# Optimization experiments

Hardware: AMD Instinct MI355X
Metric: run time of the kernel (lower is better)

Reference implementation:

```python
import jax, jax.numpy as jnp
import numpy as np
from jax import lax


def setup_inputs() -> dict:
    key = jax.random.key(0)
    kx, kw = jax.random.split(key)
    x = jax.random.normal(kx, (8, 32, 16, 160, 160), dtype=jnp.float32)
    # xavier-normal-ish init (scale irrelevant to correctness testing)
    weights = jax.random.normal(kw, (32, 32, 1, 3, 3), dtype=jnp.float32) * 0.1
    return {"x": x, "weights": weights}


def reference(x, weights):
    # per-(out_ch, in_ch) scale: mean |w| over kernel dims (2,3,4), detached
    scale = lax.stop_gradient(jnp.mean(jnp.abs(weights), axis=(2, 3, 4), keepdims=True))
    binary_no_grad = scale * jnp.sign(weights)          # {+-scale}
    clipped = jnp.clip(weights, -1.0, 1.0)
    # straight-through estimator: value = binary_no_grad, grad flows via clipped
    binary_weights = lax.stop_gradient(binary_no_grad - clipped) + clipped
    out = lax.conv_general_dilated(
        x, binary_weights,
        window_strides=(1, 1, 1),
        padding=((0, 0), (1, 1), (1, 1)),
        rhs_dilation=(1, 1, 1),
        dimension_numbers=("NCDHW", "OIDHW", "NCDHW"),
        feature_group_count=1,
    )
    return out
```

## Files before the change

kernel.cpp:

```cpp
#include <hip/hip_runtime.h>


typedef _Float16 half8 __attribute__((ext_vector_type(8)));
typedef float    floatx4 __attribute__((ext_vector_type(4)));

#define DHW  409600
#define HW   25600

__global__ void bnn_wprep_kernel(const float* __restrict__ w,
                                 _Float16* __restrict__ ws) {
    const int tid = threadIdx.x;
    #pragma unroll
    for (int p4 = 0; p4 < 4; ++p4) {
        const int oi = tid * 4 + p4;
        const int o  = oi >> 5;
        const int i  = oi & 31;
        const float* wp = w + oi * 9;
        float s = 0.f;
        #pragma unroll
        for (int t = 0; t < 9; ++t) s += fabsf(wp[t]);
        s *= (1.f / 9.f);
        const int l = ((i >> 3) << 4) | (o & 15);
        const int p = o >> 4;
        const int j = i & 7;
        #pragma unroll
        for (int t = 0; t < 9; ++t) {
            const float v  = wp[t];
            const float sg = (v > 0.f) ? 1.f : ((v < 0.f) ? -1.f : 0.f);
            ws[((t * 2 + p) * 64 + l) * 8 + j] = (_Float16)(s * sg);
        }
    }
}

__global__ __launch_bounds__(512, 4) void bnn_conv3d_kernel(
        const float* __restrict__ x, const _Float16* __restrict__ ws,
        float* __restrict__ out) {
    __shared__ __align__(16) _Float16 ldsh[31104];

    const int tid  = threadIdx.x;
    const int lane = tid & 63;
    const int wid  = tid >> 6;

    const int bid = blockIdx.x;
    const int ht  = bid % 40;
    const int nd  = bid / 40;
    const int d   = nd & 15;
    const int n   = nd >> 4;
    const int h0  = ht * 4;

    float xv[8][8];
    #pragma unroll
    for (int it = 0; it < 8; ++it) {
        const bool active = (it < 7) || (tid < 256);
        const int idx  = it * 512 + tid;
        const int wpos = idx % 160;
        const int rest = idx / 160;
        const int kg   = rest & 3;
        const int r    = rest >> 2;
        const int h_in = h0 - 1 + r;
        if (active && (unsigned)h_in < 160u) {
            const float* src = x + ((n * 32 + kg * 8) * 16 + d) * HW
                                 + h_in * 160 + wpos;
            #pragma unroll
            for (int c = 0; c < 8; ++c) xv[it][c] = src[c * DHW];
        } else {
            #pragma unroll
            for (int c = 0; c < 8; ++c) xv[it][c] = 0.f;
        }
    }

    if (tid < 192) {
        const int pos = tid >> 4, word = tid & 15;
        const int r   = pos >> 1;
        const int w1  = (pos & 1) ? 161 : 0;
        reinterpret_cast<unsigned int*>(ldsh)[(r * 162 + w1) * 16 + word] = 0u;
    }

    #pragma unroll
    for (int it = 0; it < 8; ++it) {
        const bool active = (it < 7) || (tid < 256);
        if (active) {
            const int idx  = it * 512 + tid;
            const int wpos = idx % 160;
            const int rest = idx / 160;
            const int kg   = rest & 3;
            const int r    = rest >> 2;
            half8 pk;
            #pragma unroll
            for (int c = 0; c < 8; ++c) pk[c] = (_Float16)xv[it][c];
            const int w1  = wpos + 1;
            const int skg = kg ^ ((w1 >> 1) & 3);
            *reinterpret_cast<half8*>(&ldsh[(r * 162 + w1) * 32 + skg * 8]) = pk;
        }
    }
    __syncthreads();

    half8 wf[2][9];
    {
        const half8* fb = reinterpret_cast<const half8*>(ws);
        #pragma unroll
        for (int t = 0; t < 9; ++t) {
            wf[0][t] = fb[(t * 2 + 0) * 64 + lane];
            wf[1][t] = fb[(t * 2 + 1) * 64 + lane];
        }
    }

    const int s16   = lane & 15;
    const int kg    = lane >> 4;
    const int row   = wid & 3;
    const int whalf = wid >> 2;
    const int h     = h0 + row;
    const int obase = (n * 32 + s16) * DHW + d * HW + h * 160 + kg * 4;

    #pragma unroll
    for (int wtl = 0; wtl < 5; ++wtl) {
        const int wbase = (whalf * 5 + wtl) * 16;
        floatx4 acc0 = {0.f, 0.f, 0.f, 0.f};
        floatx4 acc1 = {0.f, 0.f, 0.f, 0.f};
        #pragma unroll
        for (int kh = 0; kh < 3; ++kh) {
            const int rrow = (row + kh) * 162;
            #pragma unroll
            for (int kw = 0; kw < 3; ++kw) {
                const int w1   = wbase + s16 + kw;
                const int aidx = (rrow + w1) * 32 + ((kg ^ ((w1 >> 1) & 3)) * 8);
                const half8 a  = *reinterpret_cast<const half8*>(&ldsh[aidx]);
                const int t = kh * 3 + kw;
                acc0 = __builtin_amdgcn_mfma_f32_16x16x32_f16(a, wf[0][t], acc0, 0, 0, 0);
                acc1 = __builtin_amdgcn_mfma_f32_16x16x32_f16(a, wf[1][t], acc1, 0, 0, 0);
            }
        }
        float* op = out + obase + wbase;
        *reinterpret_cast<floatx4*>(op)            = acc0;
        *reinterpret_cast<floatx4*>(op + 16 * DHW) = acc1;
    }
}

extern "C" void kernel_launch(void* const* d_in, const int* in_sizes, int n_in,
                              void* d_out, int out_size, void* d_ws, size_t ws_size,
                              hipStream_t stream) {
    const float* x = (const float*)d_in[0];
    const float* w = (const float*)d_in[1];
    float* out = (float*)d_out;
    _Float16* ws = (_Float16*)d_ws;
    bnn_wprep_kernel<<<dim3(1), dim3(256), 0, stream>>>(w, ws);
    bnn_conv3d_kernel<<<dim3(5120), dim3(512), 0, stream>>>(x, ws, out);
}
```

Baseline: 229.0 us.

## Vectorize input loads to float4 and re-swizzle LDS layout for conflict-free writes

Each thread now loads 4 consecutive w positions per channel with float4 global loads (2 items per thread instead of 8 scalar groups), then writes 4 half8 vectors to LDS. The LDS swizzle gains an extra XOR on the w index to avoid bank conflicts from the new write pattern. Weight fragment loads move before the barrier so they overlap with the staging, and the MFMA loop is reordered kw-outer to hoist address math. This aims to cut global load instruction count and LDS conflicts, at the cost of more registers held across the barrier.

```diff
diff --git a/kernel.cpp b/kernel.cpp
--- a/kernel.cpp
+++ b/kernel.cpp
@@ -6,6 +6,12 @@
 
 #define DHW  409600
 #define HW   25600
+
+__device__ __forceinline__ int lds_half_idx(int r, int w1, int kg) {
+    const int w1x = w1 ^ ((w1 >> 2) & 1);
+    const int skg = kg ^ (((w1 >> 1) ^ (w1 >> 3)) & 3);
+    return (r * 162 + w1x) * 32 + skg * 8;
+}
 
 __global__ void bnn_wprep_kernel(const float* __restrict__ w,
                                  _Float16* __restrict__ ws) {
@@ -48,25 +54,33 @@
     const int n   = nd >> 4;
     const int h0  = ht * 4;
 
-    float xv[8][8];
-    #pragma unroll
-    for (int it = 0; it < 8; ++it) {
-        const bool active = (it < 7) || (tid < 256);
-        const int idx  = it * 512 + tid;
-        const int wpos = idx % 160;
-        const int rest = idx / 160;
-        const int kg   = rest & 3;
-        const int r    = rest >> 2;
-        const int h_in = h0 - 1 + r;
-        if (active && (unsigned)h_in < 160u) {
-            const float* src = x + ((n * 32 + kg * 8) * 16 + d) * HW
-                                 + h_in * 160 + wpos;
-            #pragma unroll
-            for (int c = 0; c < 8; ++c) xv[it][c] = src[c * DHW];
-        } else {
-            #pragma unroll
-            for (int c = 0; c < 8; ++c) xv[it][c] = 0.f;
-        }
+    const int  wq0 = tid % 40;
+    const int  rs0 = tid / 40;
+    const int  kg0 = rs0 & 3;
+    const int  r0  = rs0 >> 2;
+    const int  hi0 = h0 - 1 + r0;
+    const bool v0l = (unsigned)hi0 < 160u;
+
+    const bool act1 = tid < 448;
+    const int  id1  = tid + 512;
+    const int  wq1 = id1 % 40;
+    const int  rs1 = id1 / 40;
+    const int  kg1 = rs1 & 3;
+    const int  r1  = rs1 >> 2;
+    const int  hi1 = h0 - 1 + r1;
+    const bool v1l = act1 && ((unsigned)hi1 < 160u);
+
+    floatx4 fl0[8], fl1[8];
+    {
+        const floatx4 z = {0.f, 0.f, 0.f, 0.f};
+        const float* s0 = x + ((n * 32 + kg0 * 8) * 16 + d) * HW + hi0 * 160 + wq0 * 4;
+        const float* s1 = x + ((n * 32 + kg1 * 8) * 16 + d) * HW + hi1 * 160 + wq1 * 4;
+        #pragma unroll
+        for (int c = 0; c < 8; ++c)
+            fl0[c] = v0l ? *reinterpret_cast<const floatx4*>(s0 + c * DHW) : z;
+        #pragma unroll
+        for (int c = 0; c < 8; ++c)
+            fl1[c] = v1l ? *reinterpret_cast<const floatx4*>(s1 + c * DHW) : z;
     }
 
     if (tid < 192) {
@@ -76,24 +90,26 @@
         reinterpret_cast<unsigned int*>(ldsh)[(r * 162 + w1) * 16 + word] = 0u;
     }
 
+    __builtin_amdgcn_sched_barrier(0);
+
     #pragma unroll
-    for (int it = 0; it < 8; ++it) {
-        const bool active = (it < 7) || (tid < 256);
-        if (active) {
-            const int idx  = it * 512 + tid;
-            const int wpos = idx % 160;
-            const int rest = idx / 160;
-            const int kg   = rest & 3;
-            const int r    = rest >> 2;
+    for (int u = 0; u < 4; ++u) {
+        half8 pk;
+        #pragma unroll
+        for (int c = 0; c < 8; ++c) pk[c] = (_Float16)fl0[c][u];
+        const int w1 = wq0 * 4 + 1 + u;
+        *reinterpret_cast<half8*>(&ldsh[lds_half_idx(r0, w1, kg0)]) = pk;
+    }
+    if (act1) {
+        #pragma unroll
+        for (int u = 0; u < 4; ++u) {
             half8 pk;
             #pragma unroll
-            for (int c = 0; c < 8; ++c) pk[c] = (_Float16)xv[it][c];
-            const int w1  = wpos + 1;
-            const int skg = kg ^ ((w1 >> 1) & 3);
-            *reinterpret_cast<half8*>(&ldsh[(r * 162 + w1) * 32 + skg * 8]) = pk;
+            for (int c = 0; c < 8; ++c) pk[c] = (_Float16)fl1[c][u];
+            const int w1 = wq1 * 4 + 1 + u;
+            *reinterpret_cast<half8*>(&ldsh[lds_half_idx(r1, w1, kg1)]) = pk;
         }
     }
-    __syncthreads();
 
     half8 wf[2][9];
     {
@@ -104,6 +120,7 @@
             wf[1][t] = fb[(t * 2 + 1) * 64 + lane];
         }
     }
+    __syncthreads();
 
     const int s16   = lane & 15;
     const int kg    = lane >> 4;
@@ -118,13 +135,14 @@
         floatx4 acc0 = {0.f, 0.f, 0.f, 0.f};
         floatx4 acc1 = {0.f, 0.f, 0.f, 0.f};
         #pragma unroll
-        for (int kh = 0; kh < 3; ++kh) {
-            const int rrow = (row + kh) * 162;
+        for (int kw = 0; kw < 3; ++kw) {
+            const int w1  = wbase + s16 + kw;
+            const int w1x = w1 ^ ((w1 >> 2) & 1);
+            const int sub = ((kg ^ (((w1 >> 1) ^ (w1 >> 3)) & 3)) * 8) + w1x * 32;
             #pragma unroll
-            for (int kw = 0; kw < 3; ++kw) {
-                const int w1   = wbase + s16 + kw;
-                const int aidx = (rrow + w1) * 32 + ((kg ^ ((w1 >> 1) & 3)) * 8);
-                const half8 a  = *reinterpret_cast<const half8*>(&ldsh[aidx]);
+            for (int kh = 0; kh < 3; ++kh) {
+                const half8 a = *reinterpret_cast<const half8*>(
+                        &ldsh[(row + kh) * (162 * 32) + sub]);
                 const int t = kh * 3 + kw;
                 acc0 = __builtin_amdgcn_mfma_f32_16x16x32_f16(a, wf[0][t], acc0, 0, 0, 0);
                 acc1 = __builtin_amdgcn_mfma_f32_16x16x32_f16(a, wf[1][t], acc1, 0, 0, 0);
```

New measurement: 206.0 us. 1.11x faster.
